# Performance work log

Measured on AMD Instinct MI355X. Metric: run time of the kernel, lower is better.

## Reference

```python
import jax, jax.numpy as jnp
import numpy as np

H, W = 512, 1024
NUM_CLASSES = 19
N_THING = 8
CENTER_THRESHOLD = 0.1
NMS_KERNEL = 7
KEEP_K = 128


def setup_inputs() -> dict:
    key = jax.random.key(0)
    k1, k2, k3 = jax.random.split(key, 3)
    return {
        "semantic_logits": jax.random.normal(k1, (1, H, W, NUM_CLASSES), jnp.float32),
        "center_heatmap": jax.random.uniform(k2, (H, W, 1), dtype=jnp.float32),
        "center_offsets": jax.random.normal(k3, (H, W, 2), jnp.float32) * 8.0,
        "thing_class_ids": jnp.arange(N_THING, dtype=jnp.int32),
    }


def _nms_heatmap(center_heatmap):
    # threshold, then keep only local maxima of a k x k max-pool (zero-padded;
    # -inf init is equivalent since thresholded values are >= 0)
    hm = jnp.where(center_heatmap > CENTER_THRESHOLD, center_heatmap, 0.0)  # [H,W,1]
    pooled = jax.lax.reduce_window(hm, -jnp.inf, jax.lax.max,
                                   (NMS_KERNEL, NMS_KERNEL, 1), (1, 1, 1), 'SAME')
    hm = jnp.where(pooled == hm, hm, 0.0)
    return hm[..., 0]  # [H,W]


def reference(semantic_logits, center_heatmap, center_offsets, thing_class_ids):
    # semantic prediction [H,W] (batch=1, like the TF merge path)
    semantic = jnp.argmax(semantic_logits, axis=-1).astype(jnp.int32)[0]
    thing_mask = (semantic[..., None] == thing_class_ids[None, None, :]).any(-1)  # [H,W] bool

    hm = _nms_heatmap(center_heatmap)                     # [H,W]
    scores, idx = jax.lax.top_k(hm.reshape(-1), KEEP_K)   # fixed-K centers
    valid = scores > 0.0                                  # [K]
    cy = (idx // W).astype(jnp.float32)
    cx = (idx % W).astype(jnp.float32)
    centers = jnp.stack([cy, cx], axis=-1)                # [K,2] (y,x)

    # center-per-pixel = pixel coord + predicted offset
    yy, xx = jnp.meshgrid(jnp.arange(H, dtype=jnp.float32),
                          jnp.arange(W, dtype=jnp.float32), indexing='ij')
    cpp = (jnp.stack([yy, xx], axis=-1) + center_offsets).reshape(-1, 2)  # [HW,2]

    # squared euclidean distance (argmin-equivalent to tf.norm), matmul form
    d2 = ((centers ** 2).sum(-1)[:, None]
          - 2.0 * centers @ cpp.T
          + (cpp ** 2).sum(-1)[None, :])                  # [K,HW]
    d2 = jnp.where(valid[:, None], d2, jnp.inf)           # mask padded centers
    assign = jnp.argmin(d2, axis=0).reshape(H, W)         # closest center index

    instance_seg = (assign.astype(jnp.int32) + 1) * thing_mask.astype(jnp.int32)
    score_map = scores[assign] * thing_mask.astype(jnp.float32)
    return instance_seg, hm, score_map, semantic
```

## Files before the change

### kernel.cpp

```cpp
#include <hip/hip_runtime.h>

#define HH 512
#define WW 1024
#define HWSZ (HH*WW)
#define NCLS 19
#define KEEP 128
#define CTHR 0.1f
#define NBLK 512
#define NRED 16
#define SEGPB 32
#define GSLOT 192
typedef unsigned long long u64;

static __device__ __forceinline__ int key_bin(u64 k) {
    unsigned u = (unsigned)(k >> 32);
    if (u >= 0x3F000000u) {
        int b = 4096 + (int)((u - 0x3F000000u) >> 11);
        return b > 8191 ? 8191 : b;
    }
    return (int)(u >> 19);
}

static __device__ __forceinline__ int lds_push(int* cnt, bool want, int lane, u64 lmask_lt) {
    u64 mask = __ballot(want);
    int pos = -1;
    if (mask) {
        int leader = __builtin_ctzll(mask);
        int bpos = 0;
        if (lane == leader) bpos = atomicAdd(cnt, (int)__popcll(mask));
        bpos = __shfl(bpos, leader);
        if (want) pos = bpos + (int)__popcll(mask & lmask_lt);
    }
    return pos;
}

static __device__ __forceinline__ void bitonic_lds(u64* b, int m, int tid) {
    for (int kk = 2; kk <= m; kk <<= 1) {
        for (int j = kk >> 1; j; j >>= 1) {
            for (int i = tid; i < m; i += 256) {
                int ixj = i ^ j;
                if (ixj > i) {
                    bool desc = ((i & kk) == 0);
                    u64 a = b[i], c = b[ixj];
                    if ((a < c) == desc) { b[i] = c; b[ixj] = a; }
                }
            }
            __syncthreads();
        }
    }
}

static __device__ __forceinline__ void bitonic256_reg(u64* ov, int tid) {
    u64 a = ov[tid];
    __syncthreads();
    for (int kk = 2; kk <= 256; kk <<= 1) {
        bool desc = ((tid & kk) == 0);
        for (int j = kk >> 1; j; j >>= 1) {
            u64 b;
            if (j >= 64) {
                ov[tid] = a; __syncthreads();
                b = ov[tid ^ j]; __syncthreads();
            } else {
                b = __shfl_xor(a, j);
            }
            bool up = ((tid & j) == 0);
            bool keepMax = (up == desc);
            a = keepMax ? (a > b ? a : b) : (a < b ? a : b);
        }
    }
    ov[tid] = a;
    __syncthreads();
}

static __device__ __forceinline__ void find_cutoff(unsigned* hist, unsigned* cs, int K,
                                                   int tid, int* s_bin, int* s_chunk, unsigned* s_cabove) {
    if (tid == 0) { *s_bin = 8192; *s_chunk = -1; }
    unsigned c = 0;
    for (int i = 0; i < 32; i++) c += hist[tid * 32 + i];
    cs[tid] = c;
    __syncthreads();
    for (int d = 1; d < 256; d <<= 1) {
        unsigned v = cs[tid];
        unsigned w = (tid + d < 256) ? cs[tid + d] : 0u;
        __syncthreads();
        cs[tid] = v + w;
        __syncthreads();
    }
    unsigned above = (tid < 255) ? cs[tid + 1] : 0u;
    unsigned incl = cs[tid];
    if (K > 0 && above < (unsigned)K && (unsigned)K <= incl) { *s_chunk = tid; *s_cabove = above; }
    __syncthreads();
    if (tid < 64 && *s_chunk >= 0) {
        int ch = *s_chunk;
        unsigned v = (tid < 32) ? hist[ch * 32 + tid] : 0u;
        unsigned s = v;
        for (int d = 1; d < 64; d <<= 1) {
            unsigned o = __shfl_down(s, d);
            if (tid + d < 64) s += o;
        }
        unsigned ab = *s_cabove + (s - v);
        if (tid < 32 && ab < (unsigned)K && (unsigned)K <= *s_cabove + s)
            *s_bin = ch * 32 + tid;
    }
    __syncthreads();
}

__global__ void nms_kernel(const float* __restrict__ hm_in, float* __restrict__ hm_out,
                           u64* __restrict__ keys, int* __restrict__ blkcnt, int maxpb)
{
    const int TX = 64, TY = 16;
    __shared__ float sin_[TY + 6][TX + 6];
    __shared__ float shm[TY + 6][TX];
    __shared__ u64 lkeys[TX * TY];
    __shared__ int lcnt;

    if (threadIdx.x == 0) lcnt = 0;
    int bx = blockIdx.x & 15, by = blockIdx.x >> 4;
    int ox = bx * TX, oy = by * TY;

    for (int i = threadIdx.x; i < (TY + 6) * (TX + 6); i += blockDim.x) {
        int ly = i / (TX + 6), lx = i % (TX + 6);
        int gy = oy + ly - 3, gx = ox + lx - 3;
        float v = 0.f;
        if (gy >= 0 && gy < HH && gx >= 0 && gx < WW) {
            float t = hm_in[gy * WW + gx];
            v = (t > CTHR) ? t : 0.f;
        }
        sin_[ly][lx] = v;
    }
    __syncthreads();
    for (int i = threadIdx.x; i < (TY + 6) * TX; i += blockDim.x) {
        int ly = i / TX, lx = i % TX;
        float m = sin_[ly][lx];
#pragma unroll
        for (int d = 1; d < 7; d++) m = fmaxf(m, sin_[ly][lx + d]);
        shm[ly][lx] = m;
    }
    __syncthreads();
    for (int i = threadIdx.x; i < TY * TX; i += blockDim.x) {
        int ly = i / TX, lx = i % TX;
        float m = shm[ly][lx];
#pragma unroll
        for (int d = 1; d < 7; d++) m = fmaxf(m, shm[ly + d][lx]);
        float c = sin_[ly + 3][lx + 3];
        float o = (m == c) ? c : 0.f;
        int gy = oy + ly, gx = ox + lx;
        hm_out[gy * WW + gx] = o;
        if (o > 0.f) {
            int pos = atomicAdd(&lcnt, 1);
            lkeys[pos] = ((u64)__float_as_uint(o) << 32) |
                         (u64)(0xFFFFFFFFu - (unsigned)(gy * WW + gx));
        }
    }
    __syncthreads();
    int n = lcnt < maxpb ? lcnt : maxpb;
    if (threadIdx.x == 0) blkcnt[blockIdx.x] = n;
    for (int i = threadIdx.x; i < n; i += blockDim.x)
        keys[(size_t)i * NBLK + blockIdx.x] = lkeys[i];
}

__global__ void __launch_bounds__(256) reduce_kernel(const u64* __restrict__ keys,
                                                     const int* __restrict__ blkcnt, int maxpb,
                                                     u64* __restrict__ gtop, int* __restrict__ gcnt)
{
    __shared__ __align__(16) char smem[64512];
    u64* kbuf = (u64*)smem;
    unsigned* hist = (unsigned*)(smem + 30720);
    u64* ov = (u64*)(smem + 30720);
    unsigned* cs = (unsigned*)(smem + 63488);
    __shared__ int scnt[SEGPB];
    __shared__ int s_n, s_m, s_bin, s_chunk;
    __shared__ unsigned s_cabove;

    int tid = threadIdx.x, lane = tid & 63;
    u64 lmask_lt = (1ull << lane) - 1ull;
    int g0 = blockIdx.x * SEGPB;

    if (tid < SEGPB) {
        int c = blkcnt[g0 + tid];
        scnt[tid] = c < 0 ? 0 : (c > maxpb ? maxpb : c);
    }
    if (tid == 0) { s_n = 0; s_m = 0; }
    {
        uint4* h4 = (uint4*)hist;
        for (int i = tid; i < 2048; i += 256) h4[i] = make_uint4(0, 0, 0, 0);
    }
    __syncthreads();
    int mxc = 0;
    for (int j = 0; j < SEGPB; j++) { int c = scnt[j]; mxc = c > mxc ? c : mxc; }

    int iters = (SEGPB * mxc + 255) >> 8;
    for (int it = 0; it < iters; ++it) {
        int i = it * 256 + tid;
        int sg = i & (SEGPB - 1), sl = i >> 5;
        bool pv = (sl < scnt[sg]);
        u64 kv = pv ? keys[(size_t)sl * NBLK + (g0 + sg)] : 0ull;
        int pos = lds_push(&s_n, pv, lane, lmask_lt);
        if (pv) kbuf[pos] = kv;
    }
    __syncthreads();
    int tcnt = s_n;
    int K = tcnt < KEEP ? tcnt : KEEP;

    for (int i = tid; i < tcnt; i += 256) atomicAdd(&hist[key_bin(kbuf[i])], 1u);
    __syncthreads();

    find_cutoff(hist, cs, K, tid, &s_bin, &s_chunk, &s_cabove);
    int cb = s_bin;

    int citers = (tcnt + 255) >> 8;
    for (int it = 0; it < citers; ++it) {
        int i = it * 256 + tid;
        bool want = (i < tcnt) && key_bin(kbuf[i]) >= cb;
        int pos = lds_push(&s_m, want, lane, lmask_lt);
        if (want) ov[pos] = kbuf[i];
    }
    __syncthreads();
    int n = s_m;
    if (n <= GSLOT) {
        if (tid == 0) gcnt[blockIdx.x] = n;
        for (int i = tid; i < n; i += 256) gtop[blockIdx.x * GSLOT + i] = ov[i];
    } else {
        int m = 256; while (m < n) m <<= 1;
        for (int i = tid; i < m; i += 256) if (i >= n) ov[i] = 0ull;
        __syncthreads();
        if (m == 256) bitonic256_reg(ov, tid); else bitonic_lds(ov, m, tid);
        if (tid == 0) gcnt[blockIdx.x] = KEEP;
        if (tid < KEEP) gtop[blockIdx.x * GSLOT + tid] = ov[tid];
    }
}

__global__ void __launch_bounds__(256) select_kernel(const u64* __restrict__ gtop,
                                                     const int* __restrict__ gcnt,
                                                     float4* __restrict__ centers)
{
    __shared__ __align__(16) char smem[58368];
    u64* kbuf = (u64*)smem;
    unsigned* hist = (unsigned*)(smem + 24576);
    u64* ov = (u64*)(smem + 24576);
    unsigned* cs = (unsigned*)(smem + 57344);
    __shared__ int scnt[NRED];
    __shared__ int s_n, s_m, s_bin, s_chunk;
    __shared__ unsigned s_cabove;

    int tid = threadIdx.x, lane = tid & 63;
    u64 lmask_lt = (1ull << lane) - 1ull;

    if (tid < NRED) {
        int c = gcnt[tid];
        scnt[tid] = c < 0 ? 0 : (c > GSLOT ? GSLOT : c);
    }
    if (tid == 0) { s_n = 0; s_m = 0; }
    {
        uint4* h4 = (uint4*)hist;
        for (int i = tid; i < 2048; i += 256) h4[i] = make_uint4(0, 0, 0, 0);
    }
    __syncthreads();

    for (int it = 0; it < (NRED * GSLOT) / 256; ++it) {
        int i = it * 256 + tid;
        int b = i / GSLOT, j = i % GSLOT;
        bool pv = (j < scnt[b]);
        u64 kv = pv ? gtop[i] : 0ull;
        int pos = lds_push(&s_n, pv, lane, lmask_lt);
        if (pv) kbuf[pos] = kv;
    }
    __syncthreads();
    int tcnt = s_n;
    int K = tcnt < KEEP ? tcnt : KEEP;

    for (int i = tid; i < tcnt; i += 256) atomicAdd(&hist[key_bin(kbuf[i])], 1u);
    __syncthreads();

    find_cutoff(hist, cs, K, tid, &s_bin, &s_chunk, &s_cabove);
    int cb = s_bin;

    int citers = (tcnt + 255) >> 8;
    for (int it = 0; it < citers; ++it) {
        int i = it * 256 + tid;
        bool want = (i < tcnt) && key_bin(kbuf[i]) >= cb;
        int pos = lds_push(&s_m, want, lane, lmask_lt);
        if (want) ov[pos] = kbuf[i];
    }
    __syncthreads();
    int n = s_m;
    int m = 256; while (m < n) m <<= 1;
    for (int i = tid; i < m; i += 256) if (i >= n) ov[i] = 0ull;
    __syncthreads();
    if (m == 256) bitonic256_reg(ov, tid); else bitonic_lds(ov, m, tid);

    if (tid < KEEP) {
        u64 k64 = ov[tid];
        float sc_, cy, cx, a;
        if (k64 == 0ull) { sc_ = 0.f; cy = 0.f; cx = 0.f; a = 0.f; }
        else {
            sc_ = __uint_as_float((unsigned)(k64 >> 32));
            unsigned idx = 0xFFFFFFFFu - (unsigned)(k64 & 0xFFFFFFFFu);
            cy = (float)(idx / WW);
            cx = (float)(idx % WW);
            a = cy * cy + cx * cx;
        }
        centers[tid] = make_float4(cy, cx, a, sc_);
    }
}

__global__ void __launch_bounds__(256) assign_kernel(
        const float* __restrict__ logits, const float* __restrict__ offs,
        const int* __restrict__ thing_ids, int n_thing,
        const float4* __restrict__ centers, float* __restrict__ out)
{
    __shared__ float4 sc[KEEP];
    __shared__ float4 skept[KEEP];
    __shared__ int   skidx[KEEP];
    __shared__ float slog[256 * NCLS];
    __shared__ float sred[16];
    __shared__ float ured[4];
    __shared__ int   wcnt[4];
    __shared__ int   s_nkept;
    __shared__ int   sids[32];

    int tid = threadIdx.x;
    if (tid < KEEP) sc[tid] = centers[tid];
    if (tid < n_thing) sids[tid] = thing_ids[tid];

    int bx = blockIdx.x & 63;
    int by = blockIdx.x >> 6;
    int lr = tid >> 4, lc = tid & 15;
    int gy = by * 16 + lr, gx = bx * 16 + lc;
    int p  = gy * WW + gx;

    {
        const float4* src4 = (const float4*)(logits + ((size_t)(by * 16) * WW + bx * 16) * NCLS);
        float4* dst4 = (float4*)slog;
        for (int i = tid; i < 16 * 76; i += 256) {
            int r = i / 76, c = i % 76;
            dst4[i] = src4[(size_t)r * 4864 + c];
        }
    }

    float2 off2 = ((const float2*)offs)[p];
    float py = __fadd_rn((float)gy, off2.x);
    float px = __fadd_rn((float)gx, off2.y);

    float ymn = py, ymx = py, xmn = px, xmx = px;
    for (int d = 32; d; d >>= 1) {
        ymn = fminf(ymn, __shfl_xor(ymn, d));
        ymx = fmaxf(ymx, __shfl_xor(ymx, d));
        xmn = fminf(xmn, __shfl_xor(xmn, d));
        xmx = fmaxf(xmx, __shfl_xor(xmx, d));
    }
    if ((tid & 63) == 0) {
        int w = tid >> 6;
        sred[w * 4 + 0] = ymn; sred[w * 4 + 1] = ymx;
        sred[w * 4 + 2] = xmn; sred[w * 4 + 3] = xmx;
    }
    __syncthreads();

    ymn = fminf(fminf(sred[0], sred[4]), fminf(sred[8],  sred[12]));
    ymx = fmaxf(fmaxf(sred[1], sred[5]), fmaxf(sred[9],  sred[13]));
    xmn = fminf(fminf(sred[2], sred[6]), fminf(sred[10], sred[14]));
    xmx = fmaxf(fmaxf(sred[3], sred[7]), fmaxf(sred[11], sred[15]));

    float L = INFINITY, U = INFINITY;
    bool valid = false;
    if (tid < KEEP) {
        float4 c4 = sc[tid];
        valid = (c4.w > 0.f);
        if (valid) {
            float dyl = fmaxf(fmaxf(ymn - c4.x, c4.x - ymx), 0.f);
            float dxl = fmaxf(fmaxf(xmn - c4.y, c4.y - xmx), 0.f);
            L = dyl * dyl + dxl * dxl;
            float dyu = fmaxf(fabsf(c4.x - ymn), fabsf(c4.x - ymx));
            float dxu = fmaxf(fabsf(c4.y - xmn), fabsf(c4.y - xmx));
            U = dyu * dyu + dxu * dxu;
        }
    }
    float u = U;
    for (int d = 32; d; d >>= 1) u = fminf(u, __shfl_xor(u, d));
    if ((tid & 63) == 0) ured[tid >> 6] = u;
    __syncthreads();
    float Umin = fminf(fminf(ured[0], ured[1]), fminf(ured[2], ured[3]));

    bool keep = valid && (L <= Umin + 8.0f);
    u64 mask = __ballot(keep);
    int lane = tid & 63;
    int prefix = __popcll(mask & ((1ull << lane) - 1ull));
    if (lane == 0) wcnt[tid >> 6] = __popcll(mask);
    __syncthreads();
    int base = (tid >> 6) == 1 ? wcnt[0] : 0;
    if (keep) { skept[base + prefix] = sc[tid]; skidx[base + prefix] = tid; }
    if (tid == 0) s_nkept = wcnt[0] + wcnt[1];
    __syncthreads();

    const float* l = slog + tid * NCLS;
    float best = l[0];
    int cls = 0;
#pragma unroll
    for (int c = 1; c < NCLS; c++) {
        float v = l[c];
        if (v > best) { best = v; cls = c; }
    }
    bool thing = false;
    for (int j = 0; j < n_thing; j++) thing = thing || (cls == sids[j]);

    float b = __fadd_rn(__fmul_rn(py, py), __fmul_rn(px, px));

    float bestd = INFINITY;
    int bi = -1;
    int nk = s_nkept;
    for (int k = 0; k < nk; k++) {
        float4 c4 = skept[k];
        float m  = __fmaf_rn(c4.y, px, __fmul_rn(c4.x, py));
        float d2 = __fadd_rn(__fsub_rn(c4.z, __fadd_rn(m, m)), b);
        if (d2 < bestd) { bestd = d2; bi = k; }
    }

    float inst, smap;
    if (bi < 0) { inst = thing ? 1.f : 0.f; smap = 0.f; }
    else {
        inst = thing ? (float)(skidx[bi] + 1) : 0.f;
        smap = thing ? skept[bi].w : 0.f;
    }
    out[p] = inst;
    out[2 * HWSZ + p] = smap;
    out[3 * HWSZ + p] = (float)cls;
}

extern "C" void kernel_launch(void* const* d_in, const int* in_sizes, int n_in,
                              void* d_out, int out_size, void* d_ws, size_t ws_size,
                              hipStream_t stream) {
    const float* logits = (const float*)d_in[0];
    const float* heat   = (const float*)d_in[1];
    const float* offs   = (const float*)d_in[2];
    const int*   tids   = (const int*)d_in[3];
    int n_thing = in_sizes[3];
    if (n_thing > 32) n_thing = 32;

    float* out = (float*)d_out;
    char* ws = (char*)d_ws;
    int* blkcnt = (int*)ws;
    int* gcnt = (int*)(ws + 2048);
    float4* centers = (float4*)(ws + 4096);
    u64* gtop = (u64*)(ws + 8192);
    long long avail = (long long)ws_size - 32768;
    int maxpb = (int)(avail / (NBLK * 8));
    if (maxpb > 120) maxpb = 120;
    if (maxpb < 16) maxpb = 16;
    u64* keys = (u64*)(ws + 32768);

    nms_kernel<<<dim3(NBLK), dim3(256), 0, stream>>>(heat, out + HWSZ, keys, blkcnt, maxpb);
    reduce_kernel<<<dim3(NRED), dim3(256), 0, stream>>>(keys, blkcnt, maxpb, gtop, gcnt);
    select_kernel<<<dim3(1), dim3(256), 0, stream>>>(gtop, gcnt, centers);
    assign_kernel<<<dim3((WW / 16) * (HH / 16)), dim3(256), 0, stream>>>(logits, offs, tids, n_thing, centers, out);
}
```

Baseline: 47.57 us.

## Fuse top-K selection into assign kernel with a single winner block and flag spin-wait

Replaces the two-stage reduce/select kernels and the separate assign kernel with one fused kernel. One block, claimed by atomicCAS, performs a single-pass histogram top-K over all NMS keys and publishes the centers through a global flag. The other blocks load their logits tile and compute bounding boxes, then spin on the flag before the distance step. This removes two kernel launches and the intermediate gtop round trip, and overlaps the logits loads with the selection. The cost is a serial selection running in one block, plus a cross-block spin wait that relies on the winner block being scheduled, which risks stalls.

Result: slower. 96.04 us (+101.9%).

```diff
diff --git a/kernel.cpp b/kernel.cpp
--- a/kernel.cpp
+++ b/kernel.cpp
@@ -7,9 +7,6 @@
 #define KEEP 128
 #define CTHR 0.1f
 #define NBLK 512
-#define NRED 16
-#define SEGPB 32
-#define GSLOT 192
 typedef unsigned long long u64;
 
 static __device__ __forceinline__ int key_bin(u64 k) {
@@ -72,41 +69,9 @@
     __syncthreads();
 }
 
-static __device__ __forceinline__ void find_cutoff(unsigned* hist, unsigned* cs, int K,
-                                                   int tid, int* s_bin, int* s_chunk, unsigned* s_cabove) {
-    if (tid == 0) { *s_bin = 8192; *s_chunk = -1; }
-    unsigned c = 0;
-    for (int i = 0; i < 32; i++) c += hist[tid * 32 + i];
-    cs[tid] = c;
-    __syncthreads();
-    for (int d = 1; d < 256; d <<= 1) {
-        unsigned v = cs[tid];
-        unsigned w = (tid + d < 256) ? cs[tid + d] : 0u;
-        __syncthreads();
-        cs[tid] = v + w;
-        __syncthreads();
-    }
-    unsigned above = (tid < 255) ? cs[tid + 1] : 0u;
-    unsigned incl = cs[tid];
-    if (K > 0 && above < (unsigned)K && (unsigned)K <= incl) { *s_chunk = tid; *s_cabove = above; }
-    __syncthreads();
-    if (tid < 64 && *s_chunk >= 0) {
-        int ch = *s_chunk;
-        unsigned v = (tid < 32) ? hist[ch * 32 + tid] : 0u;
-        unsigned s = v;
-        for (int d = 1; d < 64; d <<= 1) {
-            unsigned o = __shfl_down(s, d);
-            if (tid + d < 64) s += o;
-        }
-        unsigned ab = *s_cabove + (s - v);
-        if (tid < 32 && ab < (unsigned)K && (unsigned)K <= *s_cabove + s)
-            *s_bin = ch * 32 + tid;
-    }
-    __syncthreads();
-}
-
 __global__ void nms_kernel(const float* __restrict__ hm_in, float* __restrict__ hm_out,
-                           u64* __restrict__ keys, int* __restrict__ blkcnt, int maxpb)
+                           u64* __restrict__ keys, int* __restrict__ blkcnt, int maxpb,
+                           int* __restrict__ claimp, int* __restrict__ flagp)
 {
     const int TX = 64, TY = 16;
     __shared__ float sin_[TY + 6][TX + 6];
@@ -114,6 +79,7 @@
     __shared__ u64 lkeys[TX * TY];
     __shared__ int lcnt;
 
+    if (blockIdx.x == 0 && threadIdx.x == 0) { *claimp = 0; *flagp = 0; }
     if (threadIdx.x == 0) lcnt = 0;
     int bx = blockIdx.x & 15, by = blockIdx.x >> 4;
     int ox = bx * TX, oy = by * TY;
@@ -159,182 +125,149 @@
         keys[(size_t)i * NBLK + blockIdx.x] = lkeys[i];
 }
 
-__global__ void __launch_bounds__(256) reduce_kernel(const u64* __restrict__ keys,
-                                                     const int* __restrict__ blkcnt, int maxpb,
-                                                     u64* __restrict__ gtop, int* __restrict__ gcnt)
+__global__ void __launch_bounds__(256) fused_kernel(
+        const float* __restrict__ logits, const float* __restrict__ offs,
+        const int* __restrict__ thing_ids, int n_thing,
+        const u64* __restrict__ keys, const int* __restrict__ blkcnt, int maxpb,
+        float4* __restrict__ centers, int* __restrict__ claimp, int* __restrict__ flagp,
+        float* __restrict__ out)
 {
-    __shared__ __align__(16) char smem[64512];
-    u64* kbuf = (u64*)smem;
-    unsigned* hist = (unsigned*)(smem + 30720);
-    u64* ov = (u64*)(smem + 30720);
-    unsigned* cs = (unsigned*)(smem + 63488);
-    __shared__ int scnt[SEGPB];
-    __shared__ int s_n, s_m, s_bin, s_chunk;
+    __shared__ __align__(16) char smem[35904];
+    __shared__ int s_win, s_n, s_m, s_bin, s_chunk, s_K, s_nkept;
     __shared__ unsigned s_cabove;
-
-    int tid = threadIdx.x, lane = tid & 63;
+    __shared__ float sred[16];
+    __shared__ float ured[4];
+    __shared__ int wcnt[4];
+    __shared__ int sids[32];
+
+    int tid = threadIdx.x, lane = tid & 63, wid = tid >> 6;
     u64 lmask_lt = (1ull << lane) - 1ull;
-    int g0 = blockIdx.x * SEGPB;
-
-    if (tid < SEGPB) {
-        int c = blkcnt[g0 + tid];
-        scnt[tid] = c < 0 ? 0 : (c > maxpb ? maxpb : c);
-    }
-    if (tid == 0) { s_n = 0; s_m = 0; }
-    {
-        uint4* h4 = (uint4*)hist;
-        for (int i = tid; i < 2048; i += 256) h4[i] = make_uint4(0, 0, 0, 0);
-    }
-    __syncthreads();
-    int mxc = 0;
-    for (int j = 0; j < SEGPB; j++) { int c = scnt[j]; mxc = c > mxc ? c : mxc; }
-
-    int iters = (SEGPB * mxc + 255) >> 8;
-    for (int it = 0; it < iters; ++it) {
-        int i = it * 256 + tid;
-        int sg = i & (SEGPB - 1), sl = i >> 5;
-        bool pv = (sl < scnt[sg]);
-        u64 kv = pv ? keys[(size_t)sl * NBLK + (g0 + sg)] : 0ull;
-        int pos = lds_push(&s_n, pv, lane, lmask_lt);
-        if (pv) kbuf[pos] = kv;
-    }
-    __syncthreads();
-    int tcnt = s_n;
-    int K = tcnt < KEEP ? tcnt : KEEP;
-
-    for (int i = tid; i < tcnt; i += 256) atomicAdd(&hist[key_bin(kbuf[i])], 1u);
-    __syncthreads();
-
-    find_cutoff(hist, cs, K, tid, &s_bin, &s_chunk, &s_cabove);
-    int cb = s_bin;
-
-    int citers = (tcnt + 255) >> 8;
-    for (int it = 0; it < citers; ++it) {
-        int i = it * 256 + tid;
-        bool want = (i < tcnt) && key_bin(kbuf[i]) >= cb;
-        int pos = lds_push(&s_m, want, lane, lmask_lt);
-        if (want) ov[pos] = kbuf[i];
-    }
-    __syncthreads();
-    int n = s_m;
-    if (n <= GSLOT) {
-        if (tid == 0) gcnt[blockIdx.x] = n;
-        for (int i = tid; i < n; i += 256) gtop[blockIdx.x * GSLOT + i] = ov[i];
-    } else {
+
+    if (tid == 0) s_win = (blockIdx.x < 64) ? (atomicCAS(claimp, 0, 1) == 0) : 0;
+    if (tid < n_thing) sids[tid] = thing_ids[tid];
+    __syncthreads();
+
+    if (s_win) {
+        int* scnt = (int*)smem;
+        unsigned* hist = (unsigned*)(smem + 2048);
+        u64* ov = (u64*)(smem + 2048);
+        unsigned* cs = (unsigned*)(smem + 34816);
+        if (tid == 0) { s_n = 0; s_m = 0; s_bin = 8192; s_chunk = -1; }
+        int c0 = blkcnt[2 * tid];  c0 = c0 < 0 ? 0 : (c0 > maxpb ? maxpb : c0);
+        int c1 = blkcnt[2 * tid + 1]; c1 = c1 < 0 ? 0 : (c1 > maxpb ? maxpb : c1);
+        scnt[2 * tid] = c0; scnt[2 * tid + 1] = c1;
+        int mx = c0 > c1 ? c0 : c1;
+        for (int d = 32; d; d >>= 1) { int o = __shfl_xor(mx, d); mx = mx > o ? mx : o; }
+        if (lane == 0) wcnt[wid] = mx;
+        { uint4* h4 = (uint4*)hist; for (int i = tid; i < 2048; i += 256) h4[i] = make_uint4(0,0,0,0); }
+        __syncthreads();
+        int m01 = wcnt[0] > wcnt[1] ? wcnt[0] : wcnt[1];
+        int m23 = wcnt[2] > wcnt[3] ? wcnt[2] : wcnt[3];
+        int maxc = m01 > m23 ? m01 : m23;
+        int iters = (maxc * NBLK + 1023) >> 10;
+
+        for (int it = 0; it < iters; ++it) {
+            u64 kv[4]; bool pv[4];
+#pragma unroll
+            for (int u = 0; u < 4; u++) {
+                int i = it * 1024 + u * 256 + tid;
+                int sg = i & (NBLK - 1), sl = i >> 9;
+                pv[u] = (sl < scnt[sg]);
+                kv[u] = pv[u] ? keys[(size_t)sl * NBLK + sg] : 0ull;
+            }
+#pragma unroll
+            for (int u = 0; u < 4; u++)
+                if (pv[u]) atomicAdd(&hist[key_bin(kv[u])], 1u);
+        }
+        __syncthreads();
+
+        unsigned c = 0;
+        for (int i = 0; i < 32; i++) c += hist[tid * 32 + i];
+        cs[tid] = c;
+        __syncthreads();
+        for (int d = 1; d < 256; d <<= 1) {
+            unsigned v = cs[tid];
+            unsigned w = (tid + d < 256) ? cs[tid + d] : 0u;
+            __syncthreads();
+            cs[tid] = v + w;
+            __syncthreads();
+        }
+        if (tid == 0) s_K = (int)cs[0] < KEEP ? (int)cs[0] : KEEP;
+        __syncthreads();
+        int K = s_K;
+        unsigned above = (tid < 255) ? cs[tid + 1] : 0u;
+        if (K > 0 && above < (unsigned)K && (unsigned)K <= cs[tid]) { s_chunk = tid; s_cabove = above; }
+        __syncthreads();
+        if (tid < 64 && s_chunk >= 0) {
+            int ch = s_chunk;
+            unsigned v = (tid < 32) ? hist[ch * 32 + tid] : 0u;
+            unsigned s = v;
+            for (int d = 1; d < 64; d <<= 1) {
+                unsigned o = __shfl_down(s, d);
+                if (tid + d < 64) s += o;
+            }
+            unsigned ab = s_cabove + (s - v);
+            if (tid < 32 && ab < (unsigned)K && (unsigned)K <= s_cabove + s)
+                s_bin = ch * 32 + tid;
+        }
+        __syncthreads();
+        int cb = s_bin;
+
+        for (int it = 0; it < iters; ++it) {
+#pragma unroll
+            for (int u = 0; u < 4; u++) {
+                int i = it * 1024 + u * 256 + tid;
+                int sg = i & (NBLK - 1), sl = i >> 9;
+                bool pv = (sl < scnt[sg]);
+                u64 kv = pv ? keys[(size_t)sl * NBLK + sg] : 0ull;
+                bool want = pv && key_bin(kv) >= cb;
+                int pos = lds_push(&s_m, want, lane, lmask_lt);
+                if (want && pos < 2048) ov[pos] = kv;
+            }
+        }
+        __syncthreads();
+        int n = s_m; if (n > 2048) n = 2048;
         int m = 256; while (m < n) m <<= 1;
         for (int i = tid; i < m; i += 256) if (i >= n) ov[i] = 0ull;
         __syncthreads();
         if (m == 256) bitonic256_reg(ov, tid); else bitonic_lds(ov, m, tid);
-        if (tid == 0) gcnt[blockIdx.x] = KEEP;
-        if (tid < KEEP) gtop[blockIdx.x * GSLOT + tid] = ov[tid];
-    }
-}
-
-__global__ void __launch_bounds__(256) select_kernel(const u64* __restrict__ gtop,
-                                                     const int* __restrict__ gcnt,
-                                                     float4* __restrict__ centers)
-{
-    __shared__ __align__(16) char smem[58368];
-    u64* kbuf = (u64*)smem;
-    unsigned* hist = (unsigned*)(smem + 24576);
-    u64* ov = (u64*)(smem + 24576);
-    unsigned* cs = (unsigned*)(smem + 57344);
-    __shared__ int scnt[NRED];
-    __shared__ int s_n, s_m, s_bin, s_chunk;
-    __shared__ unsigned s_cabove;
-
-    int tid = threadIdx.x, lane = tid & 63;
-    u64 lmask_lt = (1ull << lane) - 1ull;
-
-    if (tid < NRED) {
-        int c = gcnt[tid];
-        scnt[tid] = c < 0 ? 0 : (c > GSLOT ? GSLOT : c);
-    }
-    if (tid == 0) { s_n = 0; s_m = 0; }
-    {
-        uint4* h4 = (uint4*)hist;
-        for (int i = tid; i < 2048; i += 256) h4[i] = make_uint4(0, 0, 0, 0);
-    }
-    __syncthreads();
-
-    for (int it = 0; it < (NRED * GSLOT) / 256; ++it) {
-        int i = it * 256 + tid;
-        int b = i / GSLOT, j = i % GSLOT;
-        bool pv = (j < scnt[b]);
-        u64 kv = pv ? gtop[i] : 0ull;
-        int pos = lds_push(&s_n, pv, lane, lmask_lt);
-        if (pv) kbuf[pos] = kv;
-    }
-    __syncthreads();
-    int tcnt = s_n;
-    int K = tcnt < KEEP ? tcnt : KEEP;
-
-    for (int i = tid; i < tcnt; i += 256) atomicAdd(&hist[key_bin(kbuf[i])], 1u);
-    __syncthreads();
-
-    find_cutoff(hist, cs, K, tid, &s_bin, &s_chunk, &s_cabove);
-    int cb = s_bin;
-
-    int citers = (tcnt + 255) >> 8;
-    for (int it = 0; it < citers; ++it) {
-        int i = it * 256 + tid;
-        bool want = (i < tcnt) && key_bin(kbuf[i]) >= cb;
-        int pos = lds_push(&s_m, want, lane, lmask_lt);
-        if (want) ov[pos] = kbuf[i];
-    }
-    __syncthreads();
-    int n = s_m;
-    int m = 256; while (m < n) m <<= 1;
-    for (int i = tid; i < m; i += 256) if (i >= n) ov[i] = 0ull;
-    __syncthreads();
-    if (m == 256) bitonic256_reg(ov, tid); else bitonic_lds(ov, m, tid);
-
-    if (tid < KEEP) {
-        u64 k64 = ov[tid];
-        float sc_, cy, cx, a;
-        if (k64 == 0ull) { sc_ = 0.f; cy = 0.f; cx = 0.f; a = 0.f; }
-        else {
-            sc_ = __uint_as_float((unsigned)(k64 >> 32));
-            unsigned idx = 0xFFFFFFFFu - (unsigned)(k64 & 0xFFFFFFFFu);
-            cy = (float)(idx / WW);
-            cx = (float)(idx % WW);
-            a = cy * cy + cx * cx;
-        }
-        centers[tid] = make_float4(cy, cx, a, sc_);
-    }
-}
-
-__global__ void __launch_bounds__(256) assign_kernel(
-        const float* __restrict__ logits, const float* __restrict__ offs,
-        const int* __restrict__ thing_ids, int n_thing,
-        const float4* __restrict__ centers, float* __restrict__ out)
-{
-    __shared__ float4 sc[KEEP];
-    __shared__ float4 skept[KEEP];
-    __shared__ int   skidx[KEEP];
-    __shared__ float slog[256 * NCLS];
-    __shared__ float sred[16];
-    __shared__ float ured[4];
-    __shared__ int   wcnt[4];
-    __shared__ int   s_nkept;
-    __shared__ int   sids[32];
-
-    int tid = threadIdx.x;
-    if (tid < KEEP) sc[tid] = centers[tid];
-    if (tid < n_thing) sids[tid] = thing_ids[tid];
-
-    int bx = blockIdx.x & 63;
-    int by = blockIdx.x >> 6;
+
+        if (tid < KEEP) {
+            u64 k64 = ov[tid];
+            float sc_, cy, cx, a;
+            if (k64 == 0ull) { sc_ = 0.f; cy = 0.f; cx = 0.f; a = 0.f; }
+            else {
+                sc_ = __uint_as_float((unsigned)(k64 >> 32));
+                unsigned idx = 0xFFFFFFFFu - (unsigned)(k64 & 0xFFFFFFFFu);
+                cy = (float)(idx / WW);
+                cx = (float)(idx % WW);
+                a = cy * cy + cx * cx;
+            }
+            centers[tid] = make_float4(cy, cx, a, sc_);
+        }
+        __threadfence();
+        __syncthreads();
+        if (tid == 0) atomicExch(flagp, 1);
+    }
+
+    float*  slog  = (float*)smem;
+    float4* sc    = (float4*)(smem + 19456);
+    float4* skept = (float4*)(smem + 21504);
+    int*    skidx = (int*)(smem + 23552);
+
+    int tile = blockIdx.x;
+    int bx = tile & 63, by = tile >> 6;
     int lr = tid >> 4, lc = tid & 15;
     int gy = by * 16 + lr, gx = bx * 16 + lc;
     int p  = gy * WW + gx;
 
+    __syncthreads();
     {
         const float4* src4 = (const float4*)(logits + ((size_t)(by * 16) * WW + bx * 16) * NCLS);
         float4* dst4 = (float4*)slog;
         for (int i = tid; i < 16 * 76; i += 256) {
-            int r = i / 76, c = i % 76;
-            dst4[i] = src4[(size_t)r * 4864 + c];
+            int r = i / 76, cidx = i % 76;
+            dst4[i] = src4[(size_t)r * 4864 + cidx];
         }
     }
 
@@ -349,11 +282,18 @@
         xmn = fminf(xmn, __shfl_xor(xmn, d));
         xmx = fmaxf(xmx, __shfl_xor(xmx, d));
     }
-    if ((tid & 63) == 0) {
-        int w = tid >> 6;
-        sred[w * 4 + 0] = ymn; sred[w * 4 + 1] = ymx;
-        sred[w * 4 + 2] = xmn; sred[w * 4 + 3] = xmx;
-    }
+    if (lane == 0) {
+        sred[wid * 4 + 0] = ymn; sred[wid * 4 + 1] = ymx;
+        sred[wid * 4 + 2] = xmn; sred[wid * 4 + 3] = xmx;
+    }
+
+    if (tid == 0) {
+        while (__hip_atomic_load(flagp, __ATOMIC_RELAXED, __HIP_MEMORY_SCOPE_AGENT) == 0)
+            __builtin_amdgcn_s_sleep(8);
+        __threadfence();
+    }
+    __syncthreads();
+    if (tid < KEEP) sc[tid] = centers[tid];
     __syncthreads();
 
     ymn = fminf(fminf(sred[0], sred[4]), fminf(sred[8],  sred[12]));
@@ -377,17 +317,16 @@
     }
     float u = U;
     for (int d = 32; d; d >>= 1) u = fminf(u, __shfl_xor(u, d));
-    if ((tid & 63) == 0) ured[tid >> 6] = u;
+    if (lane == 0) ured[wid] = u;
     __syncthreads();
     float Umin = fminf(fminf(ured[0], ured[1]), fminf(ured[2], ured[3]));
 
     bool keep = valid && (L <= Umin + 8.0f);
-    u64 mask = __ballot(keep);
-    int lane = tid & 63;
-    int prefix = __popcll(mask & ((1ull << lane) - 1ull));
-    if (lane == 0) wcnt[tid >> 6] = __popcll(mask);
-    __syncthreads();
-    int base = (tid >> 6) == 1 ? wcnt[0] : 0;
+    u64 kmask = __ballot(keep);
+    int prefix = __popcll(kmask & lmask_lt);
+    if (lane == 0) wcnt[wid] = __popcll(kmask);
+    __syncthreads();
+    int base = (wid == 1) ? wcnt[0] : 0;
     if (keep) { skept[base + prefix] = sc[tid]; skidx[base + prefix] = tid; }
     if (tid == 0) s_nkept = wcnt[0] + wcnt[1];
     __syncthreads();
@@ -396,9 +335,9 @@
     float best = l[0];
     int cls = 0;
 #pragma unroll
-    for (int c = 1; c < NCLS; c++) {
-        float v = l[c];
-        if (v > best) { best = v; cls = c; }
+    for (int cc = 1; cc < NCLS; cc++) {
+        float v = l[cc];
+        if (v > best) { best = v; cls = cc; }
     }
     bool thing = false;
     for (int j = 0; j < n_thing; j++) thing = thing || (cls == sids[j]);
@@ -439,17 +378,18 @@
     float* out = (float*)d_out;
     char* ws = (char*)d_ws;
     int* blkcnt = (int*)ws;
-    int* gcnt = (int*)(ws + 2048);
+    int* claimp = (int*)(ws + 2048);
+    int* flagp  = (int*)(ws + 2112);
     float4* centers = (float4*)(ws + 4096);
-    u64* gtop = (u64*)(ws + 8192);
     long long avail = (long long)ws_size - 32768;
     int maxpb = (int)(avail / (NBLK * 8));
     if (maxpb > 120) maxpb = 120;
     if (maxpb < 16) maxpb = 16;
     u64* keys = (u64*)(ws + 32768);
 
-    nms_kernel<<<dim3(NBLK), dim3(256), 0, stream>>>(heat, out + HWSZ, keys, blkcnt, maxpb);
-    reduce_kernel<<<dim3(NRED), dim3(256), 0, stream>>>(keys, blkcnt, maxpb, gtop, gcnt);
-    select_kernel<<<dim3(1), dim3(256), 0, stream>>>(gtop, gcnt, centers);
-    assign_kernel<<<dim3((WW / 16) * (HH / 16)), dim3(256), 0, stream>>>(logits, offs, tids, n_thing, centers, out);
-}
+    nms_kernel<<<dim3(NBLK), dim3(256), 0, stream>>>(heat, out + HWSZ, keys, blkcnt, maxpb,
+                                                     claimp, flagp);
+    fused_kernel<<<dim3(2048), dim3(256), 0, stream>>>(logits, offs, tids, n_thing,
+                                                       keys, blkcnt, maxpb,
+                                                       centers, claimp, flagp, out);
+}
```
